# Performance work log

Measured on AMD Instinct MI355X. Metric: run time of the kernel, lower is better.

The kernel has to match this reference:

```python
import jax, jax.numpy as jnp
import numpy as np

B, T, F, H, D, L = 64, 1024, 304, 304, 128, 128  # batch, enc len, feat=emb, hidden, dict_size, max_phn_num


def _init(k, sh):
    bound = 1.0 / np.sqrt(H)
    return jax.random.uniform(k, sh, jnp.float32, -bound, bound)


def setup_inputs() -> dict:
    key = jax.random.key(0)
    ks = jax.random.split(key, 12)
    return {
        "x": jax.random.normal(ks[0], (B, T, F), jnp.float32),
        "target": jax.random.randint(ks[1], (B, L, 1), 0, D),
        "emb": jax.random.normal(ks[2], (D, F), jnp.float32),
        "enc_Wih": _init(ks[3], (3 * H, F)),
        "enc_Whh": _init(ks[4], (3 * H, H)),
        "enc_bih": _init(ks[5], (3 * H,)),
        "enc_bhh": _init(ks[6], (3 * H,)),
        "dec_Wih": _init(ks[7], (3 * H, F)),
        "dec_Whh": _init(ks[8], (3 * H, H)),
        "dec_bih": _init(ks[9], (3 * H,)),
        "dec_bhh": _init(ks[10], (3 * H,)),
        "lin_W": _init(ks[11], (D, H)),
        "lin_b": jnp.zeros((D,), jnp.float32),
    }


def gru_step(h, xt, Wih, Whh, bih, bhh):
    # PyTorch GRU cell, gate order (r, z, n)
    gi = xt @ Wih.T + bih            # [B, 3H]
    gh = h @ Whh.T + bhh             # [B, 3H]
    ir, iz, innew = jnp.split(gi, 3, axis=-1)
    hr, hz, hn = jnp.split(gh, 3, axis=-1)
    r = jax.nn.sigmoid(ir + hr)
    z = jax.nn.sigmoid(iz + hz)
    n = jnp.tanh(innew + r * hn)
    return (1.0 - z) * n + z * h


def reference(x, target, emb, enc_Wih, enc_Whh, enc_bih, enc_bhh,
              dec_Wih, dec_Whh, dec_bih, dec_bhh, lin_W, lin_b):
    Bsz = x.shape[0]
    Hdim = enc_Whh.shape[1]
    Lphn = target.shape[1]

    # ---- encoder GRU over acoustic frames ----
    h0 = jnp.zeros((Bsz, Hdim), x.dtype)

    def enc_scan(h, xt):
        return gru_step(h, xt, enc_Wih, enc_Whh, enc_bih, enc_bhh), None

    h_enc, _ = jax.lax.scan(enc_scan, h0, jnp.swapaxes(x, 0, 1))

    tok0 = target[:, 0, 0]  # [B]

    def dec_scan(carry, _):
        h, tok = carry
        e = emb[tok]                                   # [B, F]
        h = gru_step(h, e, dec_Wih, dec_Whh, dec_bih, dec_bhh)
        logits = h @ lin_W.T + lin_b                   # [B, D]
        nxt = jnp.argmax(logits, axis=-1)
        return (h, nxt), logits

    _, logits = jax.lax.scan(dec_scan, (h_enc, tok0), None, length=Lphn)
    softmaxs = jnp.swapaxes(logits, 0, 1)              # [B, L, D]

    softmax_cal = softmaxs[:, :-1, :].reshape(-1, softmaxs.shape[-1])
    target_cal = target[:, 1:, :].reshape(-1)
    asr_outputs = jnp.argmax(softmaxs[:, :-1, :], axis=2)[:, :, None]
    return softmax_cal, target_cal, asr_outputs
```

## Files before the change

kernel.cpp:

```cpp
#include <hip/hip_runtime.h>
#include <cstdint>
#include <cstddef>

#define HN 304
#define G3 912
#define US 76
#define RS 228
#define NB 64
#define TSTEPS 1024
#define LDEC 127
#define DCLS 128

#define OUT_O1 1040384
#define OUT_O2 1048512

static const size_t OFF_GI   = 0;
static const size_t OFF_HG   = 239075328ull;
static const size_t OFF_SF   = 239230976ull;
static const size_t OFF_AM   = 239232000ull;
static const size_t OFF_ABRT = 239234048ull;
static const size_t OFF_TAB  = 239234304ull;
static const size_t WS_NEED  = 239701248ull;

__global__ __launch_bounds__(256) void gi_gemm(const float* __restrict__ X,
                                               const float* __restrict__ W,
                                               const float* __restrict__ bias,
                                               float* __restrict__ out)
{
    __shared__ float xs[16][68];
    __shared__ float wsm[16][68];
    const int tid = threadIdx.x;
    const int m0 = blockIdx.x * 64;
    const int n0 = blockIdx.y * 64;
    const int tx = tid & 15, ty = tid >> 4;
    const int lr = tid >> 2;
    const int lk = (tid & 3) * 4;
    float c[4][4];
#pragma unroll
    for (int i = 0; i < 4; ++i)
#pragma unroll
        for (int j = 0; j < 4; ++j) c[i][j] = 0.f;

    for (int k0 = 0; k0 < HN; k0 += 16) {
        float4 xv = *(const float4*)(X + (size_t)(m0 + lr) * HN + k0 + lk);
        float4 wv = make_float4(0.f, 0.f, 0.f, 0.f);
        if (n0 + lr < G3) wv = *(const float4*)(W + (size_t)(n0 + lr) * HN + k0 + lk);
        xs[lk + 0][lr] = xv.x; xs[lk + 1][lr] = xv.y; xs[lk + 2][lr] = xv.z; xs[lk + 3][lr] = xv.w;
        wsm[lk + 0][lr] = wv.x; wsm[lk + 1][lr] = wv.y; wsm[lk + 2][lr] = wv.z; wsm[lk + 3][lr] = wv.w;
        __syncthreads();
#pragma unroll
        for (int kk = 0; kk < 16; ++kk) {
            const float4 a4 = *(const float4*)&xs[kk][ty * 4];
            const float4 b4 = *(const float4*)&wsm[kk][tx * 4];
            c[0][0] += a4.x * b4.x; c[0][1] += a4.x * b4.y; c[0][2] += a4.x * b4.z; c[0][3] += a4.x * b4.w;
            c[1][0] += a4.y * b4.x; c[1][1] += a4.y * b4.y; c[1][2] += a4.y * b4.z; c[1][3] += a4.y * b4.w;
            c[2][0] += a4.z * b4.x; c[2][1] += a4.z * b4.y; c[2][2] += a4.z * b4.z; c[2][3] += a4.z * b4.w;
            c[3][0] += a4.w * b4.x; c[3][1] += a4.w * b4.y; c[3][2] += a4.w * b4.z; c[3][3] += a4.w * b4.w;
        }
        __syncthreads();
    }
#pragma unroll
    for (int i = 0; i < 4; ++i) {
        const int m = m0 + ty * 4 + i;
#pragma unroll
        for (int j = 0; j < 4; ++j) {
            const int n = n0 + tx * 4 + j;
            if (n < G3) out[(size_t)m * G3 + n] = c[i][j] + bias[n];
        }
    }
}

__global__ __launch_bounds__(256) void table_k(const float* __restrict__ emb,
                                               const float* __restrict__ Wih,
                                               const float* __restrict__ bih,
                                               float* __restrict__ tab)
{
    const int idx = blockIdx.x * 256 + threadIdx.x;
    const int d = idx / G3;
    const int R = idx - d * G3;
    const float4* e4 = (const float4*)(emb + (size_t)d * HN);
    const float4* w4 = (const float4*)(Wih + (size_t)R * HN);
    float acc = 0.f;
#pragma unroll
    for (int j = 0; j < 76; ++j) {
        const float4 e = e4[j], w = w4[j];
        acc += e.x * w.x; acc += e.y * w.y; acc += e.z * w.z; acc += e.w * w.w;
    }
    tab[idx] = acc + bih[R];
}

__global__ void tcal_k(const int* __restrict__ target, float* __restrict__ out)
{
    const int i = blockIdx.x * 256 + threadIdx.x;
    if (i < NB * LDEC) {
        const int b = i / LDEC;
        const int t = i - b * LDEC;
        out[OUT_O1 + i] = (float)target[b * 128 + t + 1];
    }
}

__device__ __forceinline__ void spin_ge(int* f, int tgt, int* abortf)
{
    int g = 0;
    while (__hip_atomic_load(f, __ATOMIC_RELAXED, __HIP_MEMORY_SCOPE_AGENT) < tgt) {
        if ((++g & 255) == 0) {
            if (__hip_atomic_load(abortf, __ATOMIC_RELAXED, __HIP_MEMORY_SCOPE_AGENT) != 0) return;
            if (g > (1 << 19)) {
                __hip_atomic_store(abortf, 1, __ATOMIC_RELAXED, __HIP_MEMORY_SCOPE_AGENT);
                return;
            }
        }
    }
}

__device__ __forceinline__ unsigned long long spin_tag(unsigned long long* p, int want, int* abortf)
{
    int g = 0;
    unsigned long long r;
    for (;;) {
        r = __hip_atomic_load(p, __ATOMIC_RELAXED, __HIP_MEMORY_SCOPE_AGENT);
        if ((int)(r >> 32) >= want) return r;
        if ((++g & 255) == 0) {
            if (__hip_atomic_load(abortf, __ATOMIC_RELAXED, __HIP_MEMORY_SCOPE_AGENT) != 0) return r;
            if (g > (1 << 19)) {
                __hip_atomic_store(abortf, 1, __ATOMIC_RELAXED, __HIP_MEMORY_SCOPE_AGENT);
                return r;
            }
        }
    }
}

__global__ __launch_bounds__(1024) void rnn_persist(
    const float* __restrict__ gi,
    const float* __restrict__ encWhh, const float* __restrict__ encBhh,
    const float* __restrict__ decWhh, const float* __restrict__ decBhh,
    const float* __restrict__ tab,
    const float* __restrict__ linW, const float* __restrict__ linB,
    const int* __restrict__ target,
    float* hglob, int* syncF, unsigned long long* amax, int* abortf, float* out)
{
    const int w = blockIdx.x;
    const int b = w & 63;
    const int s = w >> 6;
    const int tid = threadIdx.x;

    __shared__ alignas(16) float hbuf[HN];
    __shared__ alignas(16) float part[4][RS];
    __shared__ alignas(16) float lpart[32][9];
    __shared__ float logit_s[32];
    __shared__ float amx_v[4];
    __shared__ int   amx_i[4];

    const int ks = tid / RS;
    const int lr = tid - ks * RS;
    const bool comp = (tid < 912);
    const int g = lr / US;
    const int ul = lr - g * US;
    const int Rrow = g * HN + s * US + ul;
    const int u = s * US + tid;
    const int cq = tid / US;

    int* flags = syncF + b * 4;
    unsigned long long* amx = amax + b * 4;

    float4 wreg[19];
    if (comp) {
        const float4* wp = (const float4*)(encWhh + (size_t)Rrow * HN + (size_t)ks * US);
#pragma unroll
        for (int j = 0; j < 19; ++j) wreg[j] = wp[j];
    }
    float b_r = 0.f, b_z = 0.f, b_n = 0.f;
    if (tid < US) { b_r = encBhh[u]; b_z = encBhh[HN + u]; b_n = encBhh[2 * HN + u]; }

    for (int i = tid; i < HN; i += 1024) hbuf[i] = 0.f;
    __syncthreads();

    const float* gib = gi + (size_t)b * TSTEPS * G3;

    for (int t = 0; t < TSTEPS; ++t) {
        const int flagv = t + 1;
        const int buf = flagv & 1;
        float gr = 0.f, gz = 0.f, gn = 0.f;
        if (tid < US) {
            const float* gp = gib + (size_t)t * G3;
            gr = gp[u]; gz = gp[HN + u]; gn = gp[2 * HN + u];
        }
        if (comp) {
            const float4* hp = (const float4*)(hbuf + ks * US);
            float acc = 0.f;
#pragma unroll
            for (int j = 0; j < 19; ++j) {
                const float4 h4 = hp[j], w4 = wreg[j];
                acc += w4.x * h4.x; acc += w4.y * h4.y; acc += w4.z * h4.z; acc += w4.w * h4.w;
            }
            part[ks][lr] = acc;
        }
        __syncthreads();
        if (tid < US) {
            const float ghr = part[0][tid] + part[1][tid] + part[2][tid] + part[3][tid] + b_r;
            const float ghz = part[0][US + tid] + part[1][US + tid] + part[2][US + tid] + part[3][US + tid] + b_z;
            const float ghn = part[0][2 * US + tid] + part[1][2 * US + tid] + part[2][2 * US + tid] + part[3][2 * US + tid] + b_n;
            const float r = 1.f / (1.f + expf(-(gr + ghr)));
            const float z = 1.f / (1.f + expf(-(gz + ghz)));
            const float n = tanhf(gn + r * ghn);
            const float hnew = (1.f - z) * n + z * hbuf[u];
            hbuf[u] = hnew;
            __hip_atomic_store(&hglob[buf * NB * HN + b * HN + u], hnew,
                               __ATOMIC_RELAXED, __HIP_MEMORY_SCOPE_AGENT);
        }
        __syncthreads();
        if (tid == 0)
            __hip_atomic_store(&flags[s], flagv, __ATOMIC_RELAXED, __HIP_MEMORY_SCOPE_AGENT);
        if (tid < HN && cq != s) {
            spin_ge(&flags[cq], flagv, abortf);
            __builtin_amdgcn_s_waitcnt(0);
            hbuf[tid] = __hip_atomic_load(&hglob[buf * NB * HN + b * HN + tid],
                                          __ATOMIC_RELAXED, __HIP_MEMORY_SCOPE_AGENT);
        }
        __syncthreads();
    }

    if (comp) {
        const float4* wp = (const float4*)(decWhh + (size_t)Rrow * HN + (size_t)ks * US);
#pragma unroll
        for (int j = 0; j < 19; ++j) wreg[j] = wp[j];
    }
    if (tid < US) { b_r = decBhh[u]; b_z = decBhh[HN + u]; b_n = decBhh[2 * HN + u]; }

    int tok = target[b * 128];
    const int lrow = tid >> 3;
    const int lks = tid & 7;

    for (int t = 0; t < LDEC; ++t) {
        const int hflagv = 1025 + t;
        const int buf = hflagv & 1;
        float gr = 0.f, gz = 0.f, gn = 0.f;
        if (tid < US) {
            const float* tp = tab + (size_t)tok * G3;
            gr = tp[u]; gz = tp[HN + u]; gn = tp[2 * HN + u];
        }
        if (comp) {
            const float4* hp = (const float4*)(hbuf + ks * US);
            float acc = 0.f;
#pragma unroll
            for (int j = 0; j < 19; ++j) {
                const float4 h4 = hp[j], w4 = wreg[j];
                acc += w4.x * h4.x; acc += w4.y * h4.y; acc += w4.z * h4.z; acc += w4.w * h4.w;
            }
            part[ks][lr] = acc;
        }
        __syncthreads();
        if (tid < US) {
            const float ghr = part[0][tid] + part[1][tid] + part[2][tid] + part[3][tid] + b_r;
            const float ghz = part[0][US + tid] + part[1][US + tid] + part[2][US + tid] + part[3][US + tid] + b_z;
            const float ghn = part[0][2 * US + tid] + part[1][2 * US + tid] + part[2][2 * US + tid] + part[3][2 * US + tid] + b_n;
            const float r = 1.f / (1.f + expf(-(gr + ghr)));
            const float z = 1.f / (1.f + expf(-(gz + ghz)));
            const float n = tanhf(gn + r * ghn);
            const float hnew = (1.f - z) * n + z * hbuf[u];
            hbuf[u] = hnew;
            __hip_atomic_store(&hglob[buf * NB * HN + b * HN + u], hnew,
                               __ATOMIC_RELAXED, __HIP_MEMORY_SCOPE_AGENT);
        }
        __syncthreads();
        if (tid == 0)
            __hip_atomic_store(&flags[s], hflagv, __ATOMIC_RELAXED, __HIP_MEMORY_SCOPE_AGENT);
        if (tid < HN && cq != s) {
            spin_ge(&flags[cq], hflagv, abortf);
            __builtin_amdgcn_s_waitcnt(0);
            hbuf[tid] = __hip_atomic_load(&hglob[buf * NB * HN + b * HN + tid],
                                          __ATOMIC_RELAXED, __HIP_MEMORY_SCOPE_AGENT);
        }
        __syncthreads();

        if (tid < 256) {
            const float2* wl = (const float2*)(linW + (size_t)(s * 32 + lrow) * HN + (size_t)lks * 38);
            const float2* hl = (const float2*)(hbuf + lks * 38);
            float a = 0.f;
#pragma unroll
            for (int j = 0; j < 19; ++j) { const float2 wv = wl[j], hv = hl[j]; a += wv.x * hv.x; a += wv.y * hv.y; }
            lpart[lrow][lks] = a;
        }
        __syncthreads();
        if (tid < 32) {
            const float lg = lpart[tid][0] + lpart[tid][1] + lpart[tid][2] + lpart[tid][3]
                           + lpart[tid][4] + lpart[tid][5] + lpart[tid][6] + lpart[tid][7]
                           + linB[s * 32 + tid];
            logit_s[tid] = lg;
            out[((size_t)b * LDEC + t) * DCLS + s * 32 + tid] = lg;
        }
        __syncthreads();
        if (tid == 0) {
            float bv = logit_s[0]; int bi = 0;
            for (int i = 1; i < 32; ++i) { const float v = logit_s[i]; if (v > bv) { bv = v; bi = i; } }
            const unsigned tagf = (unsigned)(((t + 1) << 8) | (s * 32 + bi));
            const unsigned long long pk = ((unsigned long long)tagf << 32) | (unsigned long long)__float_as_uint(bv);
            __hip_atomic_store(&amx[s], pk, __ATOMIC_RELAXED, __HIP_MEMORY_SCOPE_AGENT);
        }
        if (tid < 4) {
            const unsigned long long r = spin_tag(&amx[tid], (t + 1) << 8, abortf);
            amx_v[tid] = __uint_as_float((unsigned)r);
            amx_i[tid] = (int)(r >> 32) & 255;
        }
        __syncthreads();
        {
            float gbv = amx_v[0]; int gbi = amx_i[0];
            if (amx_v[1] > gbv) { gbv = amx_v[1]; gbi = amx_i[1]; }
            if (amx_v[2] > gbv) { gbv = amx_v[2]; gbi = amx_i[2]; }
            if (amx_v[3] > gbv) { gbv = amx_v[3]; gbi = amx_i[3]; }
            tok = gbi;
            if (tid == 0 && s == 0) out[OUT_O2 + (size_t)b * LDEC + t] = (float)gbi;
        }
    }
}

extern "C" void kernel_launch(void* const* d_in, const int* in_sizes, int n_in,
                              void* d_out, int out_size, void* d_ws, size_t ws_size,
                              hipStream_t stream)
{
    (void)in_sizes; (void)n_in; (void)out_size;
    const float* x      = (const float*)d_in[0];
    const int*   target = (const int*)  d_in[1];
    const float* emb    = (const float*)d_in[2];
    const float* encWih = (const float*)d_in[3];
    const float* encWhh = (const float*)d_in[4];
    const float* encBih = (const float*)d_in[5];
    const float* encBhh = (const float*)d_in[6];
    const float* decWih = (const float*)d_in[7];
    const float* decWhh = (const float*)d_in[8];
    const float* decBih = (const float*)d_in[9];
    const float* decBhh = (const float*)d_in[10];
    const float* linW   = (const float*)d_in[11];
    const float* linB   = (const float*)d_in[12];
    float* out = (float*)d_out;
    char* ws = (char*)d_ws;

    if (ws_size < WS_NEED) return;

    float*              gi    = (float*)(ws + OFF_GI);
    float*              hglob = (float*)(ws + OFF_HG);
    int*                syncF = (int*)  (ws + OFF_SF);
    unsigned long long* amax  = (unsigned long long*)(ws + OFF_AM);
    int*                abrt  = (int*)  (ws + OFF_ABRT);
    float*              tab   = (float*)(ws + OFF_TAB);

    hipMemsetAsync(ws + OFF_ABRT, 0, 256, stream);
    gi_gemm<<<dim3(1024, 15), 256, 0, stream>>>(x, encWih, encBih, gi);
    table_k<<<456, 256, 0, stream>>>(emb, decWih, decBih, tab);
    tcal_k<<<32, 256, 0, stream>>>(target, out);
    rnn_persist<<<256, 1024, 0, stream>>>(gi, encWhh, encBhh, decWhh, decBhh, tab,
                                          linW, linB, target, hglob, syncF, amax,
                                          abrt, out);
}
```

Baseline: 3.359 ms.

## Read remote hidden-state slices directly from global in encoder matvec, drop exchange phase

In the encoder loop, each compute thread whose K-slice belongs to another block now spins on that block's flag and loads the hidden slice straight from global memory as 64-bit atomics. This replaces the separate gather into shared memory and removes one __syncthreads per step. The local slice still comes from shared memory. The change also splits accumulators for ILP, adds compiler memory barriers after the spins, and sets launch_bounds min-blocks to 4. The exchange is now spread across many threads polling flags, which risks more flag traffic and relies on the double-buffer parity staying correct without a full barrier.

```diff
diff --git a/kernel.cpp b/kernel.cpp
--- a/kernel.cpp
+++ b/kernel.cpp
@@ -111,6 +111,7 @@
             }
         }
     }
+    __asm__ volatile("" ::: "memory");
 }
 
 __device__ __forceinline__ unsigned long long spin_tag(unsigned long long* p, int want, int* abortf)
@@ -119,18 +120,23 @@
     unsigned long long r;
     for (;;) {
         r = __hip_atomic_load(p, __ATOMIC_RELAXED, __HIP_MEMORY_SCOPE_AGENT);
-        if ((int)(r >> 32) >= want) return r;
+        if ((int)(r >> 32) >= want) break;
         if ((++g & 255) == 0) {
-            if (__hip_atomic_load(abortf, __ATOMIC_RELAXED, __HIP_MEMORY_SCOPE_AGENT) != 0) return r;
+            if (__hip_atomic_load(abortf, __ATOMIC_RELAXED, __HIP_MEMORY_SCOPE_AGENT) != 0) break;
             if (g > (1 << 19)) {
                 __hip_atomic_store(abortf, 1, __ATOMIC_RELAXED, __HIP_MEMORY_SCOPE_AGENT);
-                return r;
+                break;
             }
         }
     }
-}
-
-__global__ __launch_bounds__(1024) void rnn_persist(
+    __asm__ volatile("" ::: "memory");
+    return r;
+}
+
+__device__ __forceinline__ float ull_lo(unsigned long long v) { return __uint_as_float((unsigned)v); }
+__device__ __forceinline__ float ull_hi(unsigned long long v) { return __uint_as_float((unsigned)(v >> 32)); }
+
+__global__ __launch_bounds__(1024, 4) void rnn_persist(
     const float* __restrict__ gi,
     const float* __restrict__ encWhh, const float* __restrict__ encBhh,
     const float* __restrict__ decWhh, const float* __restrict__ decBhh,
@@ -176,24 +182,40 @@
     __syncthreads();
 
     const float* gib = gi + (size_t)b * TSTEPS * G3;
+    unsigned long long* hp8base = (unsigned long long*)hglob + ((size_t)b * HN + (size_t)ks * US) / 2;
+    const size_t par8 = (size_t)NB * HN / 2;
 
     for (int t = 0; t < TSTEPS; ++t) {
-        const int flagv = t + 1;
-        const int buf = flagv & 1;
         float gr = 0.f, gz = 0.f, gn = 0.f;
         if (tid < US) {
             const float* gp = gib + (size_t)t * G3;
             gr = gp[u]; gz = gp[HN + u]; gn = gp[2 * HN + u];
         }
         if (comp) {
-            const float4* hp = (const float4*)(hbuf + ks * US);
-            float acc = 0.f;
-#pragma unroll
-            for (int j = 0; j < 19; ++j) {
-                const float4 h4 = hp[j], w4 = wreg[j];
-                acc += w4.x * h4.x; acc += w4.y * h4.y; acc += w4.z * h4.z; acc += w4.w * h4.w;
+            float acc0 = 0.f, acc1 = 0.f;
+            if (ks == s) {
+                const float4* hp = (const float4*)(hbuf + s * US);
+#pragma unroll
+                for (int j = 0; j < 19; ++j) {
+                    const float4 h4 = hp[j], w4 = wreg[j];
+                    acc0 += w4.x * h4.x; acc1 += w4.y * h4.y;
+                    acc0 += w4.z * h4.z; acc1 += w4.w * h4.w;
+                }
+            } else if (t > 0) {
+                spin_ge(&flags[ks], t, abortf);
+                unsigned long long* hp8 = hp8base + (size_t)(t & 1) * par8;
+#pragma unroll
+                for (int j = 0; j < 19; ++j) {
+                    const unsigned long long ra =
+                        __hip_atomic_load(&hp8[2 * j], __ATOMIC_RELAXED, __HIP_MEMORY_SCOPE_AGENT);
+                    const unsigned long long rb =
+                        __hip_atomic_load(&hp8[2 * j + 1], __ATOMIC_RELAXED, __HIP_MEMORY_SCOPE_AGENT);
+                    const float4 w4 = wreg[j];
+                    acc0 += w4.x * ull_lo(ra); acc1 += w4.y * ull_hi(ra);
+                    acc0 += w4.z * ull_lo(rb); acc1 += w4.w * ull_hi(rb);
+                }
             }
-            part[ks][lr] = acc;
+            part[ks][lr] = acc0 + acc1;
         }
         __syncthreads();
         if (tid < US) {
@@ -205,35 +227,34 @@
             const float n = tanhf(gn + r * ghn);
             const float hnew = (1.f - z) * n + z * hbuf[u];
             hbuf[u] = hnew;
-            __hip_atomic_store(&hglob[buf * NB * HN + b * HN + u], hnew,
+            __hip_atomic_store(&hglob[((t + 1) & 1) * NB * HN + b * HN + u], hnew,
                                __ATOMIC_RELAXED, __HIP_MEMORY_SCOPE_AGENT);
         }
         __syncthreads();
         if (tid == 0)
-            __hip_atomic_store(&flags[s], flagv, __ATOMIC_RELAXED, __HIP_MEMORY_SCOPE_AGENT);
-        if (tid < HN && cq != s) {
-            spin_ge(&flags[cq], flagv, abortf);
-            __builtin_amdgcn_s_waitcnt(0);
-            hbuf[tid] = __hip_atomic_load(&hglob[buf * NB * HN + b * HN + tid],
-                                          __ATOMIC_RELAXED, __HIP_MEMORY_SCOPE_AGENT);
-        }
-        __syncthreads();
-    }
-
+            __hip_atomic_store(&flags[s], t + 1, __ATOMIC_RELAXED, __HIP_MEMORY_SCOPE_AGENT);
+    }
+
+    if (tid < HN && cq != s) {
+        spin_ge(&flags[cq], TSTEPS, abortf);
+        hbuf[tid] = __uint_as_float((unsigned)__hip_atomic_load(
+            (unsigned int*)&hglob[0 * NB * HN + b * HN + tid],
+            __ATOMIC_RELAXED, __HIP_MEMORY_SCOPE_AGENT));
+    }
     if (comp) {
         const float4* wp = (const float4*)(decWhh + (size_t)Rrow * HN + (size_t)ks * US);
 #pragma unroll
         for (int j = 0; j < 19; ++j) wreg[j] = wp[j];
     }
     if (tid < US) { b_r = decBhh[u]; b_z = decBhh[HN + u]; b_n = decBhh[2 * HN + u]; }
-
     int tok = target[b * 128];
     const int lrow = tid >> 3;
     const int lks = tid & 7;
+    __syncthreads();
 
     for (int t = 0; t < LDEC; ++t) {
-        const int hflagv = 1025 + t;
-        const int buf = hflagv & 1;
+        const int hflagv = TSTEPS + 1 + t;
+        const int bufn = hflagv & 1;
         float gr = 0.f, gz = 0.f, gn = 0.f;
         if (tid < US) {
             const float* tp = tab + (size_t)tok * G3;
@@ -241,13 +262,14 @@
         }
         if (comp) {
             const float4* hp = (const float4*)(hbuf + ks * US);
-            float acc = 0.f;
+            float acc0 = 0.f, acc1 = 0.f;
 #pragma unroll
             for (int j = 0; j < 19; ++j) {
                 const float4 h4 = hp[j], w4 = wreg[j];
-                acc += w4.x * h4.x; acc += w4.y * h4.y; acc += w4.z * h4.z; acc += w4.w * h4.w;
+                acc0 += w4.x * h4.x; acc1 += w4.y * h4.y;
+                acc0 += w4.z * h4.z; acc1 += w4.w * h4.w;
             }
-            part[ks][lr] = acc;
+            part[ks][lr] = acc0 + acc1;
         }
         __syncthreads();
         if (tid < US) {
@@ -259,7 +281,7 @@
             const float n = tanhf(gn + r * ghn);
             const float hnew = (1.f - z) * n + z * hbuf[u];
             hbuf[u] = hnew;
-            __hip_atomic_store(&hglob[buf * NB * HN + b * HN + u], hnew,
+            __hip_atomic_store(&hglob[bufn * NB * HN + b * HN + u], hnew,
                                __ATOMIC_RELAXED, __HIP_MEMORY_SCOPE_AGENT);
         }
         __syncthreads();
@@ -267,9 +289,9 @@
             __hip_atomic_store(&flags[s], hflagv, __ATOMIC_RELAXED, __HIP_MEMORY_SCOPE_AGENT);
         if (tid < HN && cq != s) {
             spin_ge(&flags[cq], hflagv, abortf);
-            __builtin_amdgcn_s_waitcnt(0);
-            hbuf[tid] = __hip_atomic_load(&hglob[buf * NB * HN + b * HN + tid],
-                                          __ATOMIC_RELAXED, __HIP_MEMORY_SCOPE_AGENT);
+            hbuf[tid] = __uint_as_float((unsigned)__hip_atomic_load(
+                (unsigned int*)&hglob[bufn * NB * HN + b * HN + tid],
+                __ATOMIC_RELAXED, __HIP_MEMORY_SCOPE_AGENT));
         }
         __syncthreads();
 
@@ -299,7 +321,7 @@
         }
         if (tid < 4) {
             const unsigned long long r = spin_tag(&amx[tid], (t + 1) << 8, abortf);
-            amx_v[tid] = __uint_as_float((unsigned)r);
+            amx_v[tid] = ull_lo(r);
             amx_i[tid] = (int)(r >> 32) & 255;
         }
         __syncthreads();
```

Measured after the change: 8.496 ms. +152.9%, slower.

## Embed step tags in hidden-state low bits to replace flag-based cross-block sync

Applied to the files above, without the earlier changes.

Each hidden value exchanged between the four blocks of a batch row now carries a 2-bit step tag in its low mantissa bits. Consumers poll each value directly until the tag matches instead of waiting on a separate per-block flag. This removes a __syncthreads, the flag store and a dependent second global round trip per recurrent step. In exchange the two least-significant mantissa bits of the hidden state are overwritten every step, a small precision loss that compounds over 1151 recurrent steps and could flip argmax choices in the decoder.

```diff
diff --git a/kernel.cpp b/kernel.cpp
--- a/kernel.cpp
+++ b/kernel.cpp
@@ -15,12 +15,11 @@
 #define OUT_O2 1048512
 
 static const size_t OFF_GI   = 0;
-static const size_t OFF_HG   = 239075328ull;
-static const size_t OFF_SF   = 239230976ull;
-static const size_t OFF_AM   = 239232000ull;
-static const size_t OFF_ABRT = 239234048ull;
-static const size_t OFF_TAB  = 239234304ull;
-static const size_t WS_NEED  = 239701248ull;
+static const size_t OFF_HP   = 239075328ull;
+static const size_t OFF_AM   = 239230976ull;
+static const size_t OFF_ABRT = 239233024ull;
+static const size_t OFF_TAB  = 239233280ull;
+static const size_t WS_NEED  = 239700224ull;
 
 __global__ __launch_bounds__(256) void gi_gemm(const float* __restrict__ X,
                                                const float* __restrict__ W,
@@ -99,18 +98,22 @@
     }
 }
 
-__device__ __forceinline__ void spin_ge(int* f, int tgt, int* abortf)
-{
-    int g = 0;
-    while (__hip_atomic_load(f, __ATOMIC_RELAXED, __HIP_MEMORY_SCOPE_AGENT) < tgt) {
+__device__ __forceinline__ unsigned poll_tag32(unsigned int* p, unsigned want, int* abortf)
+{
+    unsigned v; int g = 0;
+    for (;;) {
+        v = __hip_atomic_load(p, __ATOMIC_RELAXED, __HIP_MEMORY_SCOPE_AGENT);
+        if ((v & 3u) == want) break;
         if ((++g & 255) == 0) {
-            if (__hip_atomic_load(abortf, __ATOMIC_RELAXED, __HIP_MEMORY_SCOPE_AGENT) != 0) return;
+            if (__hip_atomic_load(abortf, __ATOMIC_RELAXED, __HIP_MEMORY_SCOPE_AGENT) != 0) break;
             if (g > (1 << 19)) {
                 __hip_atomic_store(abortf, 1, __ATOMIC_RELAXED, __HIP_MEMORY_SCOPE_AGENT);
-                return;
+                break;
             }
         }
     }
+    __asm__ volatile("" ::: "memory");
+    return v;
 }
 
 __device__ __forceinline__ unsigned long long spin_tag(unsigned long long* p, int want, int* abortf)
@@ -119,15 +122,17 @@
     unsigned long long r;
     for (;;) {
         r = __hip_atomic_load(p, __ATOMIC_RELAXED, __HIP_MEMORY_SCOPE_AGENT);
-        if ((int)(r >> 32) >= want) return r;
+        if ((int)(r >> 32) >= want) break;
         if ((++g & 255) == 0) {
-            if (__hip_atomic_load(abortf, __ATOMIC_RELAXED, __HIP_MEMORY_SCOPE_AGENT) != 0) return r;
+            if (__hip_atomic_load(abortf, __ATOMIC_RELAXED, __HIP_MEMORY_SCOPE_AGENT) != 0) break;
             if (g > (1 << 19)) {
                 __hip_atomic_store(abortf, 1, __ATOMIC_RELAXED, __HIP_MEMORY_SCOPE_AGENT);
-                return r;
+                break;
             }
         }
     }
+    __asm__ volatile("" ::: "memory");
+    return r;
 }
 
 __global__ __launch_bounds__(1024) void rnn_persist(
@@ -137,7 +142,7 @@
     const float* __restrict__ tab,
     const float* __restrict__ linW, const float* __restrict__ linB,
     const int* __restrict__ target,
-    float* hglob, int* syncF, unsigned long long* amax, int* abortf, float* out)
+    unsigned int* hpk, unsigned long long* amax, int* abortf, float* out)
 {
     const int w = blockIdx.x;
     const int b = w & 63;
@@ -160,8 +165,8 @@
     const int u = s * US + tid;
     const int cq = tid / US;
 
-    int* flags = syncF + b * 4;
     unsigned long long* amx = amax + b * 4;
+    unsigned int* hpb = hpk + b * HN;
 
     float4 wreg[19];
     if (comp) {
@@ -178,8 +183,7 @@
     const float* gib = gi + (size_t)b * TSTEPS * G3;
 
     for (int t = 0; t < TSTEPS; ++t) {
-        const int flagv = t + 1;
-        const int buf = flagv & 1;
+        const int T = t + 1;
         float gr = 0.f, gz = 0.f, gn = 0.f;
         if (tid < US) {
             const float* gp = gib + (size_t)t * G3;
@@ -204,18 +208,15 @@
             const float z = 1.f / (1.f + expf(-(gz + ghz)));
             const float n = tanhf(gn + r * ghn);
             const float hnew = (1.f - z) * n + z * hbuf[u];
-            hbuf[u] = hnew;
-            __hip_atomic_store(&hglob[buf * NB * HN + b * HN + u], hnew,
+            const unsigned hb = (__float_as_uint(hnew) & ~3u) | ((unsigned)T & 3u);
+            hbuf[u] = __uint_as_float(hb);
+            __hip_atomic_store(&hpb[(T & 1) * NB * HN + u], hb,
                                __ATOMIC_RELAXED, __HIP_MEMORY_SCOPE_AGENT);
         }
-        __syncthreads();
-        if (tid == 0)
-            __hip_atomic_store(&flags[s], flagv, __ATOMIC_RELAXED, __HIP_MEMORY_SCOPE_AGENT);
         if (tid < HN && cq != s) {
-            spin_ge(&flags[cq], flagv, abortf);
-            __builtin_amdgcn_s_waitcnt(0);
-            hbuf[tid] = __hip_atomic_load(&hglob[buf * NB * HN + b * HN + tid],
-                                          __ATOMIC_RELAXED, __HIP_MEMORY_SCOPE_AGENT);
+            const unsigned v = poll_tag32(&hpb[(T & 1) * NB * HN + tid],
+                                          (unsigned)T & 3u, abortf);
+            hbuf[tid] = __uint_as_float(v);
         }
         __syncthreads();
     }
@@ -226,14 +227,13 @@
         for (int j = 0; j < 19; ++j) wreg[j] = wp[j];
     }
     if (tid < US) { b_r = decBhh[u]; b_z = decBhh[HN + u]; b_n = decBhh[2 * HN + u]; }
-
     int tok = target[b * 128];
     const int lrow = tid >> 3;
     const int lks = tid & 7;
+    __syncthreads();
 
     for (int t = 0; t < LDEC; ++t) {
-        const int hflagv = 1025 + t;
-        const int buf = hflagv & 1;
+        const int T = TSTEPS + 1 + t;
         float gr = 0.f, gz = 0.f, gn = 0.f;
         if (tid < US) {
             const float* tp = tab + (size_t)tok * G3;
@@ -258,18 +258,15 @@
             const float z = 1.f / (1.f + expf(-(gz + ghz)));
             const float n = tanhf(gn + r * ghn);
             const float hnew = (1.f - z) * n + z * hbuf[u];
-            hbuf[u] = hnew;
-            __hip_atomic_store(&hglob[buf * NB * HN + b * HN + u], hnew,
+            const unsigned hb = (__float_as_uint(hnew) & ~3u) | ((unsigned)T & 3u);
+            hbuf[u] = __uint_as_float(hb);
+            __hip_atomic_store(&hpb[(T & 1) * NB * HN + u], hb,
                                __ATOMIC_RELAXED, __HIP_MEMORY_SCOPE_AGENT);
         }
-        __syncthreads();
-        if (tid == 0)
-            __hip_atomic_store(&flags[s], hflagv, __ATOMIC_RELAXED, __HIP_MEMORY_SCOPE_AGENT);
         if (tid < HN && cq != s) {
-            spin_ge(&flags[cq], hflagv, abortf);
-            __builtin_amdgcn_s_waitcnt(0);
-            hbuf[tid] = __hip_atomic_load(&hglob[buf * NB * HN + b * HN + tid],
-                                          __ATOMIC_RELAXED, __HIP_MEMORY_SCOPE_AGENT);
+            const unsigned v = poll_tag32(&hpb[(T & 1) * NB * HN + tid],
+                                          (unsigned)T & 3u, abortf);
+            hbuf[tid] = __uint_as_float(v);
         }
         __syncthreads();
 
@@ -337,18 +334,16 @@
 
     if (ws_size < WS_NEED) return;
 
-    float*              gi    = (float*)(ws + OFF_GI);
-    float*              hglob = (float*)(ws + OFF_HG);
-    int*                syncF = (int*)  (ws + OFF_SF);
-    unsigned long long* amax  = (unsigned long long*)(ws + OFF_AM);
-    int*                abrt  = (int*)  (ws + OFF_ABRT);
-    float*              tab   = (float*)(ws + OFF_TAB);
-
-    hipMemsetAsync(ws + OFF_ABRT, 0, 256, stream);
+    float*              gi   = (float*)(ws + OFF_GI);
+    unsigned int*       hpk  = (unsigned int*)(ws + OFF_HP);
+    unsigned long long* amax = (unsigned long long*)(ws + OFF_AM);
+    int*                abrt = (int*)(ws + OFF_ABRT);
+    float*              tab  = (float*)(ws + OFF_TAB);
+
+    hipMemsetAsync(ws + OFF_HP, 0, OFF_TAB - OFF_HP, stream);
     gi_gemm<<<dim3(1024, 15), 256, 0, stream>>>(x, encWih, encBih, gi);
     table_k<<<456, 256, 0, stream>>>(emb, decWih, decBih, tab);
     tcal_k<<<32, 256, 0, stream>>>(target, out);
     rnn_persist<<<256, 1024, 0, stream>>>(gi, encWhh, encBhh, decWhh, decBhh, tab,
-                                          linW, linB, target, hglob, syncF, amax,
-                                          abrt, out);
-}
+                                          linW, linB, target, hpk, amax, abrt, out);
+}
```

After: 3.331 ms. About the same (-0.8%).
